# Kernel tuning notes

Measured on AMD Instinct MI355X. Metric: run time of the kernel, lower is better.

Reference implementation:

```python
import jax, jax.numpy as jnp
import numpy as np

N_HEAD = 16

def setup_inputs() -> dict:
    key = jax.random.key(0)
    ks = jax.random.split(key, 5)
    C = 1024
    x = jax.random.normal(ks[0], (2, 2048, C), dtype=jnp.float32)
    W_qkv = jax.random.normal(ks[1], (C, 3 * C), dtype=jnp.float32) * (C ** -0.5)
    b_qkv = jnp.zeros((3 * C,), dtype=jnp.float32)
    W_proj = jax.random.normal(ks[2], (C, C), dtype=jnp.float32) * (C ** -0.5)
    b_proj = jnp.zeros((C,), dtype=jnp.float32)
    return {"x": x, "W_qkv": W_qkv, "b_qkv": b_qkv, "W_proj": W_proj, "b_proj": b_proj}

def reference(x, W_qkv, b_qkv, W_proj, b_proj):
    B, T, C = x.shape
    H = N_HEAD
    D = C // H
    scale = D ** -0.5
    qkv = x @ W_qkv + b_qkv                      # [B,T,3C]
    q, k, v = jnp.split(qkv, 3, axis=-1)
    # [B,T,C] -> [B,H,T,D]
    q = q.reshape(B, T, H, D).transpose(0, 2, 1, 3)
    k = k.reshape(B, T, H, D).transpose(0, 2, 1, 3)
    v = v.reshape(B, T, H, D).transpose(0, 2, 1, 3)
    attn = jnp.einsum('bhqd,bhkd->bhqk', q, k) * scale   # [B,H,T,T]
    causal = jnp.tril(jnp.ones((T, T), dtype=bool))
    attn = jnp.where(causal, attn, -jnp.inf)
    attn = jax.nn.softmax(attn, axis=-1)
    y = jnp.einsum('bhqk,bhkd->bhqd', attn, v)           # [B,H,T,D]
    y = y.transpose(0, 2, 1, 3).reshape(B, T, C)
    return y @ W_proj + b_proj
```

## Files before the change

### kernel.cpp

```cpp
#include <hip/hip_runtime.h>

typedef __attribute__((ext_vector_type(8))) _Float16 h8;
typedef __attribute__((ext_vector_type(4))) _Float16 h4;
typedef __attribute__((ext_vector_type(2))) _Float16 h2;
typedef __attribute__((ext_vector_type(4))) float f4;
typedef __attribute__((ext_vector_type(16))) float f16v;

#define QKSCALE 0.18033688011112042f
#define Z16 {0.f,0.f,0.f,0.f,0.f,0.f,0.f,0.f,0.f,0.f,0.f,0.f,0.f,0.f,0.f,0.f}

__device__ __forceinline__ void gload16(const void* g, void* l) {
  __builtin_amdgcn_global_load_lds((const __attribute__((address_space(1))) void*)g,
                                   (__attribute__((address_space(3))) void*)l, 16, 0, 0);
}

__device__ __forceinline__ h2 pkh2(float a, float b) {
  return __builtin_bit_cast(h2, __builtin_amdgcn_cvt_pkrtz(a, b));
}
__device__ __forceinline__ h2 swap32_h2(h2 v) {
  return __builtin_bit_cast(h2, __shfl_xor(__builtin_bit_cast(int, v), 32));
}

__global__ __launch_bounds__(256) void cast_f16_kernel(const float* __restrict__ in,
                                                       _Float16* __restrict__ out, int n) {
  int i = (blockIdx.x * 256 + threadIdx.x) * 8;
  if (i >= n) return;
  const float4* p = (const float4*)(in + i);
  float4 a = p[0], b = p[1];
  h8 v;
  v[0] = (_Float16)a.x; v[1] = (_Float16)a.y; v[2] = (_Float16)a.z; v[3] = (_Float16)a.w;
  v[4] = (_Float16)b.x; v[5] = (_Float16)b.y; v[6] = (_Float16)b.z; v[7] = (_Float16)b.w;
  *(h8*)(out + i) = v;
}

__global__ __launch_bounds__(256) void transp_cast_kernel(const float* __restrict__ W,
                                                          _Float16* __restrict__ Wt, int K, int N) {
  __shared__ _Float16 tile[64][72];
  int k0 = blockIdx.y * 64, n0 = blockIdx.x * 64;
  int t = threadIdx.x;
#pragma unroll
  for (int i = 0; i < 16; ++i) {
    int idx = i * 256 + t;
    int kr = idx >> 6, nc = idx & 63;
    tile[kr][nc] = (_Float16)W[(size_t)(k0 + kr) * N + n0 + nc];
  }
  __syncthreads();
#pragma unroll
  for (int i = 0; i < 2; ++i) {
    int idx = i * 256 + t;
    int nr = idx >> 3, kc = (idx & 7) * 8;
    h8 v;
#pragma unroll
    for (int j = 0; j < 8; ++j) v[j] = tile[kc + j][nr];
    *(h8*)&Wt[(size_t)(n0 + nr) * K + k0 + kc] = v;
  }
}

template <int MODE>
__global__ __launch_bounds__(256) void gemm_f16(const _Float16* __restrict__ A,
                                                const _Float16* __restrict__ Bt,
                                                const float* __restrict__ bias,
                                                float* __restrict__ outF,
                                                _Float16* __restrict__ oQ,
                                                _Float16* __restrict__ oK,
                                                _Float16* __restrict__ oV,
                                                int M, int N, int K) {
  __shared__ _Float16 As[128 * 64];
  __shared__ _Float16 Bs[128 * 64];
  const int m0 = blockIdx.y * 128, n0 = blockIdx.x * 128;
  const int tid = threadIdx.x;
  const int wave = tid >> 6, lane = tid & 63;
  const int wr = (wave >> 1) * 64, wc = (wave & 1) * 64;
  const int lrow = lane & 15, g = lane >> 4;

  const int row_ = tid >> 3, c_ = tid & 7;

  f4 acc[4][4];
  const f4 z4 = {0.f, 0.f, 0.f, 0.f};
#pragma unroll
  for (int m = 0; m < 4; ++m)
#pragma unroll
    for (int n = 0; n < 4; ++n) acc[m][n] = z4;

  for (int k0 = 0; k0 < K; k0 += 64) {
#pragma unroll
    for (int i = 0; i < 4; ++i) {
      int row = i * 32 + row_;
      int cs = (c_ ^ (row & 7)) * 8;
      int ldst = (i * 256 + tid) * 8;
      gload16(&A[(size_t)(m0 + row) * K + k0 + cs], &As[ldst]);
      gload16(&Bt[(size_t)(n0 + row) * K + k0 + cs], &Bs[ldst]);
    }
    __syncthreads();
#pragma unroll
    for (int ss = 0; ss < 2; ++ss) {
      h8 af[4], bf[4];
#pragma unroll
      for (int m = 0; m < 4; ++m) {
        int row = wr + m * 16 + lrow;
        af[m] = *(const h8*)&As[row * 64 + (((ss * 4 + g) ^ (row & 7)) * 8)];
      }
#pragma unroll
      for (int n = 0; n < 4; ++n) {
        int row = wc + n * 16 + lrow;
        bf[n] = *(const h8*)&Bs[row * 64 + (((ss * 4 + g) ^ (row & 7)) * 8)];
      }
      __builtin_amdgcn_s_setprio(1);
#pragma unroll
      for (int m = 0; m < 4; ++m)
#pragma unroll
        for (int n = 0; n < 4; ++n)
          acc[m][n] = __builtin_amdgcn_mfma_f32_16x16x32_f16(af[m], bf[n], acc[m][n], 0, 0, 0);
      __builtin_amdgcn_s_setprio(0);
    }
    __syncthreads();
  }

#pragma unroll
  for (int n = 0; n < 4; ++n) {
    const int gcol = n0 + wc + n * 16 + lrow;
    const float bv = bias ? bias[gcol] : 0.f;
    if (MODE == 1 && (gcol >> 10) == 2) {
      const int c1 = gcol & 1023;
      const int hh = c1 >> 6, d = c1 & 63;
#pragma unroll
      for (int m = 0; m < 4; ++m) {
        const int grow = m0 + wr + m * 16 + g * 4;
        const int b = grow >> 11, t = grow & 2047;
        h4 pv;
#pragma unroll
        for (int r = 0; r < 4; ++r) pv[r] = (_Float16)(acc[m][n][r] + bv);
        *(h4*)&oV[(((size_t)(b * 16 + hh)) * 64 + d) * 2048 + t] = pv;
      }
    } else {
#pragma unroll
      for (int m = 0; m < 4; ++m) {
#pragma unroll
        for (int r = 0; r < 4; ++r) {
          const int grow = m0 + wr + m * 16 + g * 4 + r;
          float v = acc[m][n][r] + bv;
          if (MODE == 0) {
            outF[(size_t)grow * N + gcol] = v;
          } else {
            int part = gcol >> 10;
            int c1 = gcol & 1023;
            int hh = c1 >> 6, d = c1 & 63;
            int b = grow >> 11, t = grow & 2047;
            int bh = b * 16 + hh;
            if (part == 0)
              oQ[((size_t)bh * 2048 + t) * 64 + d] = (_Float16)(v * QKSCALE);
            else
              oK[((size_t)bh * 2048 + t) * 64 + d] = (_Float16)v;
          }
        }
      }
    }
  }
}

__global__ void attn_kernel(const _Float16* __restrict__ Qg,
                            const _Float16* __restrict__ Kg,
                            const _Float16* __restrict__ Vtg,
                            _Float16* __restrict__ Og) {
  __shared__ _Float16 slab[4][32][72];
  __shared__ float mlds[2][4][32];

  const int idx = blockIdx.x;
  const int bh = (idx & 7) | (((idx >> 3) & 3) << 3);
  const int pi = idx >> 5;

  const int wave = threadIdx.x >> 6, lane = threadIdx.x & 63;
  const int ln = lane & 31, hi = lane >> 5;
  const int b = bh >> 4, h = bh & 15;
  const _Float16* Q = Qg + (size_t)bh * 2048 * 64;
  const _Float16* K = Kg + (size_t)bh * 2048 * 64;
  const _Float16* Vt = Vtg + (size_t)bh * 64 * 2048;
  _Float16(*pw)[72] = slab[wave];

  for (int half = 0; half < 2; ++half) {
    const int qt2 = half == 0 ? 63 - pi : pi;
    const int q0 = qt2 * 32;

    h8 qf[4];
#pragma unroll
    for (int ds = 0; ds < 4; ++ds)
      qf[ds] = *(const h8*)&Q[(q0 + ln) * 64 + ds * 16 + hi * 8];

    f16v o0 = Z16, o1 = Z16;
    float m = -1e30f, l = 0.f;
    const int NT = qt2 + 1;

    for (int it = wave; it < NT; it += 4) {
      const int kv0 = it * 32;
      h8 kf[4];
#pragma unroll
      for (int ds = 0; ds < 4; ++ds)
        kf[ds] = *(const h8*)&K[(kv0 + ln) * 64 + ds * 16 + hi * 8];

      f16v s = Z16;
      __builtin_amdgcn_s_setprio(1);
#pragma unroll
      for (int ds = 0; ds < 4; ++ds)
        s = __builtin_amdgcn_mfma_f32_32x32x16_f16(kf[ds], qf[ds], s, 0, 0, 0);
      __builtin_amdgcn_s_setprio(0);

      h8 vf[2][2];
#pragma unroll
      for (int dt = 0; dt < 2; ++dt)
#pragma unroll
        for (int ks = 0; ks < 2; ++ks)
          vf[dt][ks] = *(const h8*)&Vt[(size_t)(dt * 32 + ln) * 2048 + kv0 + ks * 16 + hi * 8];

      if (it == NT - 1) {
#pragma unroll
        for (int reg = 0; reg < 16; ++reg) {
          const int crow = (reg & 3) + 8 * (reg >> 2) + 4 * hi;
          if (crow > ln) s[reg] = -1e30f;
        }
      }

      float pm = s[0];
#pragma unroll
      for (int reg = 1; reg < 16; ++reg) pm = fmaxf(pm, s[reg]);
      pm = fmaxf(pm, __shfl_xor(pm, 32));

      if (__any(pm > m + 8.f)) {
        const float mn = fmaxf(m, pm);
        const float fr = __builtin_amdgcn_exp2f(m - mn);
        m = mn;
        l *= fr;
#pragma unroll
        for (int reg = 0; reg < 16; ++reg) {
          const float frr = __shfl(fr, (reg & 3) + 8 * (reg >> 2) + 4 * hi);
          o0[reg] *= frr;
          o1[reg] *= frr;
        }
      }

      float ls = 0.f;
#pragma unroll
      for (int reg = 0; reg < 16; ++reg) {
        s[reg] = __builtin_amdgcn_exp2f(s[reg] - m);
        ls += s[reg];
      }
      l += ls;

      h2 Pk[4][2];
#pragma unroll
      for (int R = 0; R < 4; ++R)
#pragma unroll
        for (int pr = 0; pr < 2; ++pr)
          Pk[R][pr] = pkh2(s[4 * R + 2 * pr], s[4 * R + 2 * pr + 1]);

      __builtin_amdgcn_s_setprio(1);
#pragma unroll
      for (int ks = 0; ks < 2; ++ks) {
        const int Rb = 2 * ks;
        h2 a0p0 = Pk[Rb][0], a0p1 = Pk[Rb][1];
        h2 a1p0 = Pk[Rb + 1][0], a1p1 = Pk[Rb + 1][1];
        h2 loc0 = hi ? a1p0 : a0p0;
        h2 loc1 = hi ? a1p1 : a0p1;
        h2 snd0 = hi ? a0p0 : a1p0;
        h2 snd1 = hi ? a0p1 : a1p1;
        h2 rem0 = swap32_h2(snd0);
        h2 rem1 = swap32_h2(snd1);
        h2 w0 = hi ? rem0 : loc0;
        h2 w1 = hi ? rem1 : loc1;
        h2 w2 = hi ? loc0 : rem0;
        h2 w3 = hi ? loc1 : rem1;
        h8 pa;
        pa[0] = w0[0]; pa[1] = w0[1]; pa[2] = w1[0]; pa[3] = w1[1];
        pa[4] = w2[0]; pa[5] = w2[1]; pa[6] = w3[0]; pa[7] = w3[1];
        o0 = __builtin_amdgcn_mfma_f32_32x32x16_f16(pa, vf[0][ks], o0, 0, 0, 0);
        o1 = __builtin_amdgcn_mfma_f32_32x32x16_f16(pa, vf[1][ks], o1, 0, 0, 0);
      }
      __builtin_amdgcn_s_setprio(0);
    }

    const float l_all = l + __shfl_xor(l, 32);
    if (hi == 0) {
      mlds[0][wave][ln] = m;
      mlds[1][wave][ln] = l_all;
    }
#pragma unroll
    for (int reg = 0; reg < 16; ++reg) {
      const int crow = (reg & 3) + 8 * (reg >> 2) + 4 * hi;
      const float li = __shfl(l_all, crow);
      const float inv = li > 0.f ? 1.f / li : 0.f;
      pw[crow][ln] = (_Float16)(o0[reg] * inv);
      pw[crow][32 + ln] = (_Float16)(o1[reg] * inv);
    }
    __syncthreads();

    {
      const int ql = threadIdx.x >> 3;
      const int d0 = (threadIdx.x & 7) * 8;
      float m0 = mlds[0][0][ql], m1 = mlds[0][1][ql], m2 = mlds[0][2][ql], m3 = mlds[0][3][ql];
      float M = fmaxf(fmaxf(m0, m1), fmaxf(m2, m3));
      float f0 = __builtin_amdgcn_exp2f(m0 - M) * mlds[1][0][ql];
      float f1 = __builtin_amdgcn_exp2f(m1 - M) * mlds[1][1][ql];
      float f2 = __builtin_amdgcn_exp2f(m2 - M) * mlds[1][2][ql];
      float f3 = __builtin_amdgcn_exp2f(m3 - M) * mlds[1][3][ql];
      float inv = 1.f / (f0 + f1 + f2 + f3);
      h8 o0v = *(const h8*)&slab[0][ql][d0];
      h8 o1v = *(const h8*)&slab[1][ql][d0];
      h8 o2v = *(const h8*)&slab[2][ql][d0];
      h8 o3v = *(const h8*)&slab[3][ql][d0];
      h8 outv;
#pragma unroll
      for (int j = 0; j < 8; ++j) {
        float v = f0 * (float)o0v[j] + f1 * (float)o1v[j] + f2 * (float)o2v[j] + f3 * (float)o3v[j];
        outv[j] = (_Float16)(v * inv);
      }
      *(h8*)&Og[((size_t)b * 2048 + q0 + ql) * 1024 + h * 64 + d0] = outv;
    }
    if (half == 0) __syncthreads();
  }
}

extern "C" void kernel_launch(void* const* d_in, const int* in_sizes, int n_in,
                              void* d_out, int out_size, void* d_ws, size_t ws_size,
                              hipStream_t stream) {
  const float* x = (const float*)d_in[0];
  const float* Wqkv = (const float*)d_in[1];
  const float* bqkv = (const float*)d_in[2];
  const float* Wproj = (const float*)d_in[3];
  const float* bproj = (const float*)d_in[4];
  float* out = (float*)d_out;

  char* ws = (char*)d_ws;
  const size_t MB = 1u << 20;
  _Float16* xh     = (_Float16*)(ws + 0 * MB);
  _Float16* wqkvt  = (_Float16*)(ws + 8 * MB);
  _Float16* wprojt = (_Float16*)(ws + 14 * MB);
  _Float16* qh     = (_Float16*)(ws + 16 * MB);
  _Float16* kh     = (_Float16*)(ws + 24 * MB);
  _Float16* vth    = (_Float16*)(ws + 32 * MB);
  _Float16* oh     = (_Float16*)(ws + 40 * MB);

  cast_f16_kernel<<<2048, 256, 0, stream>>>(x, xh, 4194304);
  transp_cast_kernel<<<dim3(48, 16), 256, 0, stream>>>(Wqkv, wqkvt, 1024, 3072);
  transp_cast_kernel<<<dim3(16, 16), 256, 0, stream>>>(Wproj, wprojt, 1024, 1024);

  gemm_f16<1><<<dim3(24, 32), 256, 0, stream>>>(xh, wqkvt, bqkv, nullptr, qh, kh, vth,
                                                4096, 3072, 1024);
  attn_kernel<<<dim3(1024), 256, 0, stream>>>(qh, kh, vth, oh);
  gemm_f16<0><<<dim3(8, 32), 256, 0, stream>>>(oh, wprojt, bproj, out, nullptr, nullptr, nullptr,
                                               4096, 1024, 1024);
}
```

Baseline: 145.5 us.

## Stage K and V tiles cooperatively through LDS in attention kernel

Each 128-row KV slab is now loaded by the whole block: K goes through global_load_lds into an XOR-swizzled LDS buffer, and V^T goes through registers into a padded LDS array. Each wave then reads its own 32-row sub-tile from LDS instead of issuing its own strided global loads. The aim is coalesced global access and fewer scattered V^T row reads. The cost is two block-wide barriers per slab, which serialise the four waves and leave idle waves on the final partial slab. The output slab buffer now aliases the same shared memory.

```diff
diff --git a/kernel.cpp b/kernel.cpp
--- a/kernel.cpp
+++ b/kernel.cpp
@@ -158,24 +158,27 @@
   }
 }
 
-__global__ void attn_kernel(const _Float16* __restrict__ Qg,
-                            const _Float16* __restrict__ Kg,
-                            const _Float16* __restrict__ Vtg,
-                            _Float16* __restrict__ Og) {
-  __shared__ _Float16 slab[4][32][72];
+__global__ __launch_bounds__(256) void attn_kernel(const _Float16* __restrict__ Qg,
+                                                   const _Float16* __restrict__ Kg,
+                                                   const _Float16* __restrict__ Vtg,
+                                                   _Float16* __restrict__ Og) {
+  __shared__ __align__(16) char smem[33792];
   __shared__ float mlds[2][4][32];
+  _Float16* Kb = (_Float16*)smem;
+  _Float16(*Vb)[136] = (_Float16(*)[136])(smem + 16384);
+  _Float16(*slab)[32][72] = (_Float16(*)[32][72])smem;
 
   const int idx = blockIdx.x;
   const int bh = (idx & 7) | (((idx >> 3) & 3) << 3);
   const int pi = idx >> 5;
 
-  const int wave = threadIdx.x >> 6, lane = threadIdx.x & 63;
+  const int tid = threadIdx.x;
+  const int wave = tid >> 6, lane = tid & 63;
   const int ln = lane & 31, hi = lane >> 5;
   const int b = bh >> 4, h = bh & 15;
   const _Float16* Q = Qg + (size_t)bh * 2048 * 64;
   const _Float16* K = Kg + (size_t)bh * 2048 * 64;
   const _Float16* Vt = Vtg + (size_t)bh * 64 * 2048;
-  _Float16(*pw)[72] = slab[wave];
 
   for (int half = 0; half < 2; ++half) {
     const int qt2 = half == 0 ? 63 - pi : pi;
@@ -189,92 +192,116 @@
     f16v o0 = Z16, o1 = Z16;
     float m = -1e30f, l = 0.f;
     const int NT = qt2 + 1;
-
-    for (int it = wave; it < NT; it += 4) {
-      const int kv0 = it * 32;
-      h8 kf[4];
-#pragma unroll
-      for (int ds = 0; ds < 4; ++ds)
-        kf[ds] = *(const h8*)&K[(kv0 + ln) * 64 + ds * 16 + hi * 8];
-
-      f16v s = Z16;
-      __builtin_amdgcn_s_setprio(1);
-#pragma unroll
-      for (int ds = 0; ds < 4; ++ds)
-        s = __builtin_amdgcn_mfma_f32_32x32x16_f16(kf[ds], qf[ds], s, 0, 0, 0);
-      __builtin_amdgcn_s_setprio(0);
-
-      h8 vf[2][2];
-#pragma unroll
-      for (int dt = 0; dt < 2; ++dt)
-#pragma unroll
-        for (int ks = 0; ks < 2; ++ks)
-          vf[dt][ks] = *(const h8*)&Vt[(size_t)(dt * 32 + ln) * 2048 + kv0 + ks * 16 + hi * 8];
-
-      if (it == NT - 1) {
+    const int S = (NT + 3) >> 2;
+
+    for (int s = 0; s < S; ++s) {
+      const int kvs = s * 128;
+#pragma unroll
+      for (int i = 0; i < 4; ++i) {
+        const int L = i * 256 + tid;
+        const int row = L >> 3, c = L & 7;
+        const int cs = (c ^ (row & 7)) * 8;
+        gload16(&K[(size_t)(kvs + row) * 64 + cs], &Kb[L * 8]);
+      }
+      h8 vt[4];
+#pragma unroll
+      for (int i = 0; i < 4; ++i) {
+        const int J = i * 256 + tid;
+        const int d = J >> 4, ch = J & 15;
+        vt[i] = *(const h8*)&Vt[(size_t)d * 2048 + kvs + ch * 8];
+      }
+#pragma unroll
+      for (int i = 0; i < 4; ++i) {
+        const int J = i * 256 + tid;
+        const int d = J >> 4, ch = J & 15;
+        *(h8*)&Vb[d][ch * 8] = vt[i];
+      }
+      __syncthreads();
+
+      const int tI = s * 4 + wave;
+      if (tI < NT) {
+        const int kvloc = wave * 32;
+
+        h8 kf[4];
+#pragma unroll
+        for (int ds = 0; ds < 4; ++ds)
+          kf[ds] = *(const h8*)&Kb[wave * 2048 + ln * 64 + (((ds * 2 + hi) ^ (ln & 7)) * 8)];
+
+        f16v sv = Z16;
+        __builtin_amdgcn_s_setprio(1);
+#pragma unroll
+        for (int ds = 0; ds < 4; ++ds)
+          sv = __builtin_amdgcn_mfma_f32_32x32x16_f16(kf[ds], qf[ds], sv, 0, 0, 0);
+        __builtin_amdgcn_s_setprio(0);
+
+        if (tI == NT - 1) {
+#pragma unroll
+          for (int reg = 0; reg < 16; ++reg) {
+            const int crow = (reg & 3) + 8 * (reg >> 2) + 4 * hi;
+            if (crow > ln) sv[reg] = -1e30f;
+          }
+        }
+
+        float pm = sv[0];
+#pragma unroll
+        for (int reg = 1; reg < 16; ++reg) pm = fmaxf(pm, sv[reg]);
+        pm = fmaxf(pm, __shfl_xor(pm, 32));
+
+        if (__any(pm > m + 8.f)) {
+          const float mn = fmaxf(m, pm);
+          const float fr = __builtin_amdgcn_exp2f(m - mn);
+          m = mn;
+          l *= fr;
+#pragma unroll
+          for (int reg = 0; reg < 16; ++reg) {
+            const float frr = __shfl(fr, (reg & 3) + 8 * (reg >> 2) + 4 * hi);
+            o0[reg] *= frr;
+            o1[reg] *= frr;
+          }
+        }
+
+        float ls = 0.f;
 #pragma unroll
         for (int reg = 0; reg < 16; ++reg) {
-          const int crow = (reg & 3) + 8 * (reg >> 2) + 4 * hi;
-          if (crow > ln) s[reg] = -1e30f;
-        }
-      }
-
-      float pm = s[0];
-#pragma unroll
-      for (int reg = 1; reg < 16; ++reg) pm = fmaxf(pm, s[reg]);
-      pm = fmaxf(pm, __shfl_xor(pm, 32));
-
-      if (__any(pm > m + 8.f)) {
-        const float mn = fmaxf(m, pm);
-        const float fr = __builtin_amdgcn_exp2f(m - mn);
-        m = mn;
-        l *= fr;
-#pragma unroll
-        for (int reg = 0; reg < 16; ++reg) {
-          const float frr = __shfl(fr, (reg & 3) + 8 * (reg >> 2) + 4 * hi);
-          o0[reg] *= frr;
-          o1[reg] *= frr;
-        }
-      }
-
-      float ls = 0.f;
-#pragma unroll
-      for (int reg = 0; reg < 16; ++reg) {
-        s[reg] = __builtin_amdgcn_exp2f(s[reg] - m);
-        ls += s[reg];
-      }
-      l += ls;
-
-      h2 Pk[4][2];
-#pragma unroll
-      for (int R = 0; R < 4; ++R)
-#pragma unroll
-        for (int pr = 0; pr < 2; ++pr)
-          Pk[R][pr] = pkh2(s[4 * R + 2 * pr], s[4 * R + 2 * pr + 1]);
-
-      __builtin_amdgcn_s_setprio(1);
-#pragma unroll
-      for (int ks = 0; ks < 2; ++ks) {
-        const int Rb = 2 * ks;
-        h2 a0p0 = Pk[Rb][0], a0p1 = Pk[Rb][1];
-        h2 a1p0 = Pk[Rb + 1][0], a1p1 = Pk[Rb + 1][1];
-        h2 loc0 = hi ? a1p0 : a0p0;
-        h2 loc1 = hi ? a1p1 : a0p1;
-        h2 snd0 = hi ? a0p0 : a1p0;
-        h2 snd1 = hi ? a0p1 : a1p1;
-        h2 rem0 = swap32_h2(snd0);
-        h2 rem1 = swap32_h2(snd1);
-        h2 w0 = hi ? rem0 : loc0;
-        h2 w1 = hi ? rem1 : loc1;
-        h2 w2 = hi ? loc0 : rem0;
-        h2 w3 = hi ? loc1 : rem1;
-        h8 pa;
-        pa[0] = w0[0]; pa[1] = w0[1]; pa[2] = w1[0]; pa[3] = w1[1];
-        pa[4] = w2[0]; pa[5] = w2[1]; pa[6] = w3[0]; pa[7] = w3[1];
-        o0 = __builtin_amdgcn_mfma_f32_32x32x16_f16(pa, vf[0][ks], o0, 0, 0, 0);
-        o1 = __builtin_amdgcn_mfma_f32_32x32x16_f16(pa, vf[1][ks], o1, 0, 0, 0);
-      }
-      __builtin_amdgcn_s_setprio(0);
+          sv[reg] = __builtin_amdgcn_exp2f(sv[reg] - m);
+          ls += sv[reg];
+        }
+        l += ls;
+
+        h2 Pk[4][2];
+#pragma unroll
+        for (int R = 0; R < 4; ++R)
+#pragma unroll
+          for (int pr = 0; pr < 2; ++pr)
+            Pk[R][pr] = pkh2(sv[4 * R + 2 * pr], sv[4 * R + 2 * pr + 1]);
+
+        __builtin_amdgcn_s_setprio(1);
+#pragma unroll
+        for (int ks = 0; ks < 2; ++ks) {
+          const int Rb = 2 * ks;
+          h2 a0p0 = Pk[Rb][0], a0p1 = Pk[Rb][1];
+          h2 a1p0 = Pk[Rb + 1][0], a1p1 = Pk[Rb + 1][1];
+          h2 loc0 = hi ? a1p0 : a0p0;
+          h2 loc1 = hi ? a1p1 : a0p1;
+          h2 snd0 = hi ? a0p0 : a1p0;
+          h2 snd1 = hi ? a0p1 : a1p1;
+          h2 rem0 = swap32_h2(snd0);
+          h2 rem1 = swap32_h2(snd1);
+          h2 w0 = hi ? rem0 : loc0;
+          h2 w1 = hi ? rem1 : loc1;
+          h2 w2 = hi ? loc0 : rem0;
+          h2 w3 = hi ? loc1 : rem1;
+          h8 pa;
+          pa[0] = w0[0]; pa[1] = w0[1]; pa[2] = w1[0]; pa[3] = w1[1];
+          pa[4] = w2[0]; pa[5] = w2[1]; pa[6] = w3[0]; pa[7] = w3[1];
+          h8 vf0 = *(const h8*)&Vb[ln][kvloc + ks * 16 + hi * 8];
+          h8 vf1 = *(const h8*)&Vb[32 + ln][kvloc + ks * 16 + hi * 8];
+          o0 = __builtin_amdgcn_mfma_f32_32x32x16_f16(pa, vf0, o0, 0, 0, 0);
+          o1 = __builtin_amdgcn_mfma_f32_32x32x16_f16(pa, vf1, o1, 0, 0, 0);
+        }
+        __builtin_amdgcn_s_setprio(0);
+      }
+      __syncthreads();
     }
 
     const float l_all = l + __shfl_xor(l, 32);
@@ -282,6 +309,7 @@
       mlds[0][wave][ln] = m;
       mlds[1][wave][ln] = l_all;
     }
+    _Float16(*pw)[72] = slab[wave];
 #pragma unroll
     for (int reg = 0; reg < 16; ++reg) {
       const int crow = (reg & 3) + 8 * (reg >> 2) + 4 * hi;
@@ -293,8 +321,8 @@
     __syncthreads();
 
     {
-      const int ql = threadIdx.x >> 3;
-      const int d0 = (threadIdx.x & 7) * 8;
+      const int ql = tid >> 3;
+      const int d0 = (tid & 7) * 8;
       float m0 = mlds[0][0][ql], m1 = mlds[0][1][ql], m2 = mlds[0][2][ql], m3 = mlds[0][3][ql];
       float M = fmaxf(fmaxf(m0, m1), fmaxf(m2, m3));
       float f0 = __builtin_amdgcn_exp2f(m0 - M) * mlds[1][0][ql];
```

New measurement: 137.5 us (median of 3 runs). -5.5%, faster.
